# Performance work log

Hardware: AMD Instinct MI355X
Metric: run time of the kernel (lower is better)

Reference implementation:

```python
import jax, jax.numpy as jnp
import numpy as np

N_NODES = 50000
N_EDGES = 800000
IN_DIM = 128
HID_DIM = 128
OUT_DIM = 64


def setup_inputs() -> dict:
    key = jax.random.key(0)
    ks = jax.random.split(key, 6)
    x = jax.random.normal(ks[0], (N_NODES, IN_DIM), dtype=jnp.float32)
    row = jax.random.randint(ks[1], (N_EDGES,), 0, N_NODES, dtype=jnp.int32)
    col = jax.random.randint(ks[2], (N_EDGES,), 0, N_NODES, dtype=jnp.int32)
    vals = jax.random.uniform(ks[3], (N_EDGES,), dtype=jnp.float32)
    # Xavier-uniform init as in nn.init.xavier_uniform_
    lim1 = float(np.sqrt(6.0 / (IN_DIM + HID_DIM)))
    lim2 = float(np.sqrt(6.0 / (HID_DIM + OUT_DIM)))
    W1 = jax.random.uniform(ks[4], (IN_DIM, HID_DIM), minval=-lim1, maxval=lim1, dtype=jnp.float32)
    W2 = jax.random.uniform(ks[5], (HID_DIM, OUT_DIM), minval=-lim2, maxval=lim2, dtype=jnp.float32)
    return {"x": x, "row": row, "col": col, "vals": vals, "W1": W1, "W2": W2}


def _spmm(row, col, vals, x):
    # out[i] = sum_{e: row[e]==i} vals[e] * x[col[e]]   (sparse adj @ x)
    msgs = vals[:, None] * x[col]  # [E, D] gathered edge messages
    return jax.ops.segment_sum(msgs, row, num_segments=N_NODES)


def reference(x, row, col, vals, W1, W2):
    # GCN layer 1: adj.mm(x) -> linear -> relu  (dropout = identity in eval)
    h = jax.nn.relu(_spmm(row, col, vals, x) @ W1)
    # GCN layer 2: adj.mm(h) -> linear (no activation)
    out = _spmm(row, col, vals, h) @ W2
    return out
```

## Files before the change

kernel.cpp:

```cpp
#include <hip/hip_runtime.h>
#include <stdint.h>

#define N_NODES 50000
#define N_EDGES 800000
#define IN_DIM 128
#define HID_DIM 128
#define OUT_DIM 64

#define ELL_CAP 64
#define XCD_GROUPS 8
#define ROWS_PER_XCD (N_NODES / XCD_GROUPS)
#define SCAT_BLOCKS_PER_XCD 128

typedef short bf16x8 __attribute__((ext_vector_type(8)));
typedef float f32x4  __attribute__((ext_vector_type(4)));

__device__ __forceinline__ uint32_t pack_bf16x2(float a, float b) {
    uint32_t ba = __float_as_uint(a), bb = __float_as_uint(b);
    ba = (ba + 0x7fffu + ((ba >> 16) & 1u)) >> 16;
    bb = (bb + 0x7fffu + ((bb >> 16) & 1u)) & 0xffff0000u;
    return ba | bb;
}

__device__ __forceinline__ unsigned short f2bf(float f) {
    uint32_t u = __float_as_uint(f);
    return (unsigned short)((u + 0x7fffu + ((u >> 16) & 1u)) >> 16);
}

__device__ __forceinline__ uint32_t pack_edge(int col, float v) {
    uint32_t fb = __float_as_uint(v);
    fb = (fb + 0x7fffu + ((fb >> 16) & 1u)) & 0xffff0000u;
    return fb | (uint32_t)col;
}


__global__ __launch_bounds__(256) void zero_convert(int* __restrict__ counts,
                                                    const float* __restrict__ W1,
                                                    const float* __restrict__ W2,
                                                    unsigned short* __restrict__ wt1,
                                                    unsigned short* __restrict__ wt2) {
    int i = blockIdx.x * 256 + threadIdx.x;
    if (i < N_NODES) counts[i] = 0;
    int j = i - N_NODES;
    if (j >= 0 && j < 128 * 128) {
        int n = j >> 7, k = j & 127;
        wt1[j] = f2bf(W1[k * 128 + n]);
    }
    int l = j - 128 * 128;
    if (l >= 0 && l < 64 * 128) {
        int n = l >> 7, k = l & 127;
        wt2[l] = f2bf(W2[k * 64 + n]);
    }
}


__global__ __launch_bounds__(256) void scatter_ell(const int* __restrict__ row,
                                                   const int* __restrict__ col,
                                                   const float* __restrict__ vals,
                                                   int* __restrict__ counts,
                                                   uint32_t* __restrict__ ell) {
    const int xcd = blockIdx.x & (XCD_GROUPS - 1);
    const int blk = blockIdx.x >> 3;
    const int rlo = xcd * ROWS_PER_XCD;
    int e = blk * 256 + threadIdx.x;
    const int stride = SCAT_BLOCKS_PER_XCD * 256;
    for (; e < N_EDGES; e += stride) {
        int r = row[e];
        if ((unsigned)(r - rlo) < (unsigned)ROWS_PER_XCD) {
            int p = atomicAdd(&counts[r], 1);
            if (p < ELL_CAP)
                ell[((size_t)r << 6) + p] = pack_edge(col[e], vals[e]);
        }
    }
}


template<int N, bool AF32>
__global__ __launch_bounds__(256) void gemm_mfma(const float* __restrict__ Af,
                                                 const uint32_t* __restrict__ Apk,
                                                 const unsigned short* __restrict__ Wt,
                                                 unsigned short* __restrict__ outb) {
    const int tid = threadIdx.x;
    const int wid = tid >> 6, lane = tid & 63;
    const int l15 = lane & 15, lk = lane >> 4;
    const int n0 = blockIdx.y * 64;

    bf16x8 bfrag[4][4];
#pragma unroll
    for (int t = 0; t < 4; ++t) {
        const unsigned short* wp = Wt + (size_t)(n0 + t * 16 + l15) * 128 + lk * 8;
#pragma unroll
        for (int s = 0; s < 4; ++s)
            bfrag[t][s] = *reinterpret_cast<const bf16x8*>(wp + s * 32);
    }

    for (int mt = blockIdx.x * 4 + wid; mt < 3125; mt += 784) {
        const int row = mt * 16 + l15;
        bf16x8 afrag[4];
        if (AF32) {
            const float* ap = Af + (size_t)row * 128 + lk * 8;
#pragma unroll
            for (int s = 0; s < 4; ++s) {
                float4 p0 = *reinterpret_cast<const float4*>(ap + s * 32);
                float4 p1 = *reinterpret_cast<const float4*>(ap + s * 32 + 4);
                bf16x8 f;
                f[0] = (short)f2bf(p0.x); f[1] = (short)f2bf(p0.y);
                f[2] = (short)f2bf(p0.z); f[3] = (short)f2bf(p0.w);
                f[4] = (short)f2bf(p1.x); f[5] = (short)f2bf(p1.y);
                f[6] = (short)f2bf(p1.z); f[7] = (short)f2bf(p1.w);
                afrag[s] = f;
            }
        } else {
            const uint32_t* ap = Apk + (size_t)row * 64 + lk * 4;
#pragma unroll
            for (int s = 0; s < 4; ++s)
                afrag[s] = *reinterpret_cast<const bf16x8*>(ap + s * 16);
        }

        f32x4 acc[4] = {{0.f,0.f,0.f,0.f},{0.f,0.f,0.f,0.f},{0.f,0.f,0.f,0.f},{0.f,0.f,0.f,0.f}};
#pragma unroll
        for (int s = 0; s < 4; ++s)
#pragma unroll
            for (int t = 0; t < 4; ++t)
                acc[t] = __builtin_amdgcn_mfma_f32_16x16x32_bf16(afrag[s], bfrag[t][s], acc[t], 0, 0, 0);

#pragma unroll
        for (int t = 0; t < 4; ++t)
#pragma unroll
            for (int q = 0; q < 4; ++q) {
                int r = mt * 16 + lk * 4 + q;
                outb[(size_t)r * N + n0 + t * 16 + l15] = f2bf(acc[t][q]);
            }
    }
}


template<bool RELU>
__global__ __launch_bounds__(256) void spmm_bf16_128(const int* __restrict__ counts,
                                                     const uint32_t* __restrict__ ell,
                                                     const uint32_t* __restrict__ xp,
                                                     uint32_t* __restrict__ outp) {
    const int wid = threadIdx.x >> 6;
    const int lane = threadIdx.x & 63;
    const int r = blockIdx.x * 4 + wid;
    if (r >= N_NODES) return;
    const int start = r << 6;
    int cnt = counts[r]; if (cnt > ELL_CAP) cnt = ELL_CAP;
    const int end = start + cnt;
    const uint32_t* xb = xp + lane;

    float alo[4] = {0.f, 0.f, 0.f, 0.f};
    float ahi[4] = {0.f, 0.f, 0.f, 0.f};
    int e = start;
    for (; e + 7 < end; e += 8) {
        uint32_t c0 = ell[e],     c1 = ell[e + 1], c2 = ell[e + 2], c3 = ell[e + 3];
        uint32_t c4 = ell[e + 4], c5 = ell[e + 5], c6 = ell[e + 6], c7 = ell[e + 7];
        uint32_t u0 = xb[(size_t)(c0 & 0xffffu) * 64];
        uint32_t u1 = xb[(size_t)(c1 & 0xffffu) * 64];
        uint32_t u2 = xb[(size_t)(c2 & 0xffffu) * 64];
        uint32_t u3 = xb[(size_t)(c3 & 0xffffu) * 64];
        uint32_t u4 = xb[(size_t)(c4 & 0xffffu) * 64];
        uint32_t u5 = xb[(size_t)(c5 & 0xffffu) * 64];
        uint32_t u6 = xb[(size_t)(c6 & 0xffffu) * 64];
        uint32_t u7 = xb[(size_t)(c7 & 0xffffu) * 64];
        float v0 = __uint_as_float(c0 & 0xffff0000u), v1 = __uint_as_float(c1 & 0xffff0000u);
        float v2 = __uint_as_float(c2 & 0xffff0000u), v3 = __uint_as_float(c3 & 0xffff0000u);
        float v4 = __uint_as_float(c4 & 0xffff0000u), v5 = __uint_as_float(c5 & 0xffff0000u);
        float v6 = __uint_as_float(c6 & 0xffff0000u), v7 = __uint_as_float(c7 & 0xffff0000u);
        alo[0] = fmaf(v0, __uint_as_float(u0 << 16), alo[0]);
        ahi[0] = fmaf(v0, __uint_as_float(u0 & 0xffff0000u), ahi[0]);
        alo[1] = fmaf(v1, __uint_as_float(u1 << 16), alo[1]);
        ahi[1] = fmaf(v1, __uint_as_float(u1 & 0xffff0000u), ahi[1]);
        alo[2] = fmaf(v2, __uint_as_float(u2 << 16), alo[2]);
        ahi[2] = fmaf(v2, __uint_as_float(u2 & 0xffff0000u), ahi[2]);
        alo[3] = fmaf(v3, __uint_as_float(u3 << 16), alo[3]);
        ahi[3] = fmaf(v3, __uint_as_float(u3 & 0xffff0000u), ahi[3]);
        alo[0] = fmaf(v4, __uint_as_float(u4 << 16), alo[0]);
        ahi[0] = fmaf(v4, __uint_as_float(u4 & 0xffff0000u), ahi[0]);
        alo[1] = fmaf(v5, __uint_as_float(u5 << 16), alo[1]);
        ahi[1] = fmaf(v5, __uint_as_float(u5 & 0xffff0000u), ahi[1]);
        alo[2] = fmaf(v6, __uint_as_float(u6 << 16), alo[2]);
        ahi[2] = fmaf(v6, __uint_as_float(u6 & 0xffff0000u), ahi[2]);
        alo[3] = fmaf(v7, __uint_as_float(u7 << 16), alo[3]);
        ahi[3] = fmaf(v7, __uint_as_float(u7 & 0xffff0000u), ahi[3]);
    }
    if (e + 3 < end) {
        uint32_t c0 = ell[e], c1 = ell[e + 1], c2 = ell[e + 2], c3 = ell[e + 3];
        uint32_t u0 = xb[(size_t)(c0 & 0xffffu) * 64];
        uint32_t u1 = xb[(size_t)(c1 & 0xffffu) * 64];
        uint32_t u2 = xb[(size_t)(c2 & 0xffffu) * 64];
        uint32_t u3 = xb[(size_t)(c3 & 0xffffu) * 64];
        float v0 = __uint_as_float(c0 & 0xffff0000u), v1 = __uint_as_float(c1 & 0xffff0000u);
        float v2 = __uint_as_float(c2 & 0xffff0000u), v3 = __uint_as_float(c3 & 0xffff0000u);
        alo[0] = fmaf(v0, __uint_as_float(u0 << 16), alo[0]);
        ahi[0] = fmaf(v0, __uint_as_float(u0 & 0xffff0000u), ahi[0]);
        alo[1] = fmaf(v1, __uint_as_float(u1 << 16), alo[1]);
        ahi[1] = fmaf(v1, __uint_as_float(u1 & 0xffff0000u), ahi[1]);
        alo[2] = fmaf(v2, __uint_as_float(u2 << 16), alo[2]);
        ahi[2] = fmaf(v2, __uint_as_float(u2 & 0xffff0000u), ahi[2]);
        alo[3] = fmaf(v3, __uint_as_float(u3 << 16), alo[3]);
        ahi[3] = fmaf(v3, __uint_as_float(u3 & 0xffff0000u), ahi[3]);
        e += 4;
    }
    for (; e < end; ++e) {
        uint32_t c0 = ell[e];
        float v0 = __uint_as_float(c0 & 0xffff0000u);
        uint32_t u0 = xb[(size_t)(c0 & 0xffffu) * 64];
        alo[0] = fmaf(v0, __uint_as_float(u0 << 16), alo[0]);
        ahi[0] = fmaf(v0, __uint_as_float(u0 & 0xffff0000u), ahi[0]);
    }
    float rlo = (alo[0] + alo[1]) + (alo[2] + alo[3]);
    float rhi = (ahi[0] + ahi[1]) + (ahi[2] + ahi[3]);
    if (RELU) { rlo = fmaxf(rlo, 0.f); rhi = fmaxf(rhi, 0.f); }
    outp[(size_t)r * 64 + lane] = pack_bf16x2(rlo, rhi);
}

__global__ __launch_bounds__(256) void spmm_bf16_64(const int* __restrict__ counts,
                                                    const uint32_t* __restrict__ ell,
                                                    const uint32_t* __restrict__ xp,
                                                    float* __restrict__ out) {
    const int wid = threadIdx.x >> 6;
    const int lane = threadIdx.x & 63;
    const int r = blockIdx.x * 4 + wid;
    if (r >= N_NODES) return;
    const int start = r << 6;
    int cnt = counts[r]; if (cnt > ELL_CAP) cnt = ELL_CAP;
    const int end = start + cnt;
    const int j = lane & 31;
    const int half = lane >> 5;
    const uint32_t* xb = xp + j;

    float alo[4] = {0.f, 0.f, 0.f, 0.f};
    float ahi[4] = {0.f, 0.f, 0.f, 0.f};
    int e = start + half;
    for (; e + 6 < end; e += 8) {
        uint32_t c0 = ell[e], c1 = ell[e + 2], c2 = ell[e + 4], c3 = ell[e + 6];
        uint32_t u0 = xb[(size_t)(c0 & 0xffffu) * 32];
        uint32_t u1 = xb[(size_t)(c1 & 0xffffu) * 32];
        uint32_t u2 = xb[(size_t)(c2 & 0xffffu) * 32];
        uint32_t u3 = xb[(size_t)(c3 & 0xffffu) * 32];
        float v0 = __uint_as_float(c0 & 0xffff0000u), v1 = __uint_as_float(c1 & 0xffff0000u);
        float v2 = __uint_as_float(c2 & 0xffff0000u), v3 = __uint_as_float(c3 & 0xffff0000u);
        alo[0] = fmaf(v0, __uint_as_float(u0 << 16), alo[0]);
        ahi[0] = fmaf(v0, __uint_as_float(u0 & 0xffff0000u), ahi[0]);
        alo[1] = fmaf(v1, __uint_as_float(u1 << 16), alo[1]);
        ahi[1] = fmaf(v1, __uint_as_float(u1 & 0xffff0000u), ahi[1]);
        alo[2] = fmaf(v2, __uint_as_float(u2 << 16), alo[2]);
        ahi[2] = fmaf(v2, __uint_as_float(u2 & 0xffff0000u), ahi[2]);
        alo[3] = fmaf(v3, __uint_as_float(u3 << 16), alo[3]);
        ahi[3] = fmaf(v3, __uint_as_float(u3 & 0xffff0000u), ahi[3]);
    }
    for (; e < end; e += 2) {
        uint32_t c0 = ell[e];
        float v = __uint_as_float(c0 & 0xffff0000u);
        uint32_t u = xb[(size_t)(c0 & 0xffffu) * 32];
        alo[0] = fmaf(v, __uint_as_float(u << 16), alo[0]);
        ahi[0] = fmaf(v, __uint_as_float(u & 0xffff0000u), ahi[0]);
    }
    float alo_s = (alo[0] + alo[1]) + (alo[2] + alo[3]);
    float ahi_s = (ahi[0] + ahi[1]) + (ahi[2] + ahi[3]);
    alo_s += __shfl_xor(alo_s, 32);
    ahi_s += __shfl_xor(ahi_s, 32);
    if (half == 0) {
        float2 res = {alo_s, ahi_s};
        *reinterpret_cast<float2*>(out + (size_t)r * 64 + j * 2) = res;
    }
}


extern "C" void kernel_launch(void* const* d_in, const int* in_sizes, int n_in,
                              void* d_out, int out_size, void* d_ws, size_t ws_size,
                              hipStream_t stream) {
    const float* x    = (const float*)d_in[0];
    const int*   row  = (const int*)  d_in[1];
    const int*   col  = (const int*)  d_in[2];
    const float* vals = (const float*)d_in[3];
    const float* W1   = (const float*)d_in[4];
    const float* W2   = (const float*)d_in[5];
    float* out = (float*)d_out;

    char* ws = (char*)d_ws;
    auto align = [](size_t v) { return (v + 255) & ~(size_t)255; };
    int*      counts  = (int*)ws;              ws += align(sizeof(int) * N_NODES);
    uint32_t* ell     = (uint32_t*)ws;         ws += align(sizeof(uint32_t) * N_NODES * ELL_CAP);
    uint32_t* tpk     = (uint32_t*)ws;         ws += align(sizeof(uint32_t) * N_NODES * 64);
    uint32_t* hpk     = (uint32_t*)ws;         ws += align(sizeof(uint32_t) * N_NODES * 64);
    unsigned short* wt1 = (unsigned short*)ws; ws += align(sizeof(short) * 128 * 128);
    unsigned short* wt2 = (unsigned short*)ws; ws += align(sizeof(short) * 64 * 128);

    zero_convert<<<(N_NODES + 128 * 128 + 64 * 128 + 255) / 256, 256, 0, stream>>>(counts, W1, W2, wt1, wt2);
    scatter_ell<<<SCAT_BLOCKS_PER_XCD * XCD_GROUPS, 256, 0, stream>>>(row, col, vals, counts, ell);

    gemm_mfma<HID_DIM, true><<<dim3(196, 2), 256, 0, stream>>>(x, nullptr, wt1, (unsigned short*)tpk);
    spmm_bf16_128<true><<<(N_NODES + 3) / 4, 256, 0, stream>>>(counts, ell, tpk, hpk);

    gemm_mfma<OUT_DIM, false><<<dim3(196, 1), 256, 0, stream>>>(nullptr, hpk, wt2, (unsigned short*)tpk);
    spmm_bf16_64<<<(N_NODES + 3) / 4, 256, 0, stream>>>(counts, ell, tpk, out);
}
```

Baseline: 130.6 us.

## Fuse ELL scatter with first GEMM and store layer-1 features as FP8

Merges the edge-scatter kernel and the first MFMA GEMM into one launch by splitting the block range, so the two independent stages can run concurrently. The first GEMM now writes its output as custom FP8 (e4m3-like) bytes instead of bf16, and the first SpMM gathers 2 bytes per lane and decodes them through a shared-memory lookup table. This halves the gather traffic of the dominant sparse stage and removes one kernel launch, at the cost of reduced precision in the intermediate features and extra LDS lookups.

```diff
diff --git a/kernel.cpp b/kernel.cpp
--- a/kernel.cpp
+++ b/kernel.cpp
@@ -11,6 +11,8 @@
 #define XCD_GROUPS 8
 #define ROWS_PER_XCD (N_NODES / XCD_GROUPS)
 #define SCAT_BLOCKS_PER_XCD 128
+#define SCAT_BLOCKS (SCAT_BLOCKS_PER_XCD * XCD_GROUPS)
+#define GEMM1_BLOCKS 392
 
 typedef short bf16x8 __attribute__((ext_vector_type(8)));
 typedef float f32x4  __attribute__((ext_vector_type(4)));
@@ -25,6 +27,20 @@
 __device__ __forceinline__ unsigned short f2bf(float f) {
     uint32_t u = __float_as_uint(f);
     return (unsigned short)((u + 0x7fffu + ((u >> 16) & 1u)) >> 16);
+}
+
+__device__ __forceinline__ uint8_t f2fp8(float f) {
+    uint32_t u = __float_as_uint(f);
+    uint32_t s = (u >> 24) & 0x80u;
+    uint32_t au = u & 0x7fffffffu;
+    uint32_t r = au + 0x7FFFFu + ((au >> 20) & 1u);
+    int e = (int)((r >> 23) & 0xffu) - 120;
+    uint32_t m = (r >> 20) & 7u;
+    uint32_t out;
+    if (e <= 0) out = 0u;
+    else if (e >= 16) out = 0x7Eu;
+    else out = ((uint32_t)e << 3) | m;
+    return (uint8_t)(s | out);
 }
 
 __device__ __forceinline__ uint32_t pack_edge(int col, float v) {
@@ -54,67 +70,61 @@
 }
 
 
-__global__ __launch_bounds__(256) void scatter_ell(const int* __restrict__ row,
-                                                   const int* __restrict__ col,
-                                                   const float* __restrict__ vals,
-                                                   int* __restrict__ counts,
-                                                   uint32_t* __restrict__ ell) {
-    const int xcd = blockIdx.x & (XCD_GROUPS - 1);
-    const int blk = blockIdx.x >> 3;
-    const int rlo = xcd * ROWS_PER_XCD;
-    int e = blk * 256 + threadIdx.x;
-    const int stride = SCAT_BLOCKS_PER_XCD * 256;
-    for (; e < N_EDGES; e += stride) {
-        int r = row[e];
-        if ((unsigned)(r - rlo) < (unsigned)ROWS_PER_XCD) {
-            int p = atomicAdd(&counts[r], 1);
-            if (p < ELL_CAP)
-                ell[((size_t)r << 6) + p] = pack_edge(col[e], vals[e]);
+__global__ __launch_bounds__(256) void fused_scatter_gemm1(const int* __restrict__ row,
+                                                           const int* __restrict__ col,
+                                                           const float* __restrict__ vals,
+                                                           int* __restrict__ counts,
+                                                           uint32_t* __restrict__ ell,
+                                                           const float* __restrict__ x,
+                                                           const unsigned short* __restrict__ wt1,
+                                                           uint8_t* __restrict__ t1f8) {
+    if (blockIdx.x < SCAT_BLOCKS) {
+        const int xcd = blockIdx.x & (XCD_GROUPS - 1);
+        const int blk = blockIdx.x >> 3;
+        const int rlo = xcd * ROWS_PER_XCD;
+        int e = blk * 256 + threadIdx.x;
+        const int stride = SCAT_BLOCKS_PER_XCD * 256;
+        for (; e < N_EDGES; e += stride) {
+            int r = row[e];
+            if ((unsigned)(r - rlo) < (unsigned)ROWS_PER_XCD) {
+                int p = atomicAdd(&counts[r], 1);
+                if (p < ELL_CAP)
+                    ell[((size_t)r << 6) + p] = pack_edge(col[e], vals[e]);
+            }
         }
-    }
-}
-
-
-template<int N, bool AF32>
-__global__ __launch_bounds__(256) void gemm_mfma(const float* __restrict__ Af,
-                                                 const uint32_t* __restrict__ Apk,
-                                                 const unsigned short* __restrict__ Wt,
-                                                 unsigned short* __restrict__ outb) {
+        return;
+    }
+
+    const int g  = blockIdx.x - SCAT_BLOCKS;
+    const int bx = g % 196;
+    const int n0 = (g / 196) * 64;
     const int tid = threadIdx.x;
     const int wid = tid >> 6, lane = tid & 63;
     const int l15 = lane & 15, lk = lane >> 4;
-    const int n0 = blockIdx.y * 64;
 
     bf16x8 bfrag[4][4];
 #pragma unroll
     for (int t = 0; t < 4; ++t) {
-        const unsigned short* wp = Wt + (size_t)(n0 + t * 16 + l15) * 128 + lk * 8;
+        const unsigned short* wp = wt1 + (size_t)(n0 + t * 16 + l15) * 128 + lk * 8;
 #pragma unroll
         for (int s = 0; s < 4; ++s)
             bfrag[t][s] = *reinterpret_cast<const bf16x8*>(wp + s * 32);
     }
 
-    for (int mt = blockIdx.x * 4 + wid; mt < 3125; mt += 784) {
-        const int row = mt * 16 + l15;
+    for (int mt = bx * 4 + wid; mt < 3125; mt += 784) {
+        const int arow = mt * 16 + l15;
         bf16x8 afrag[4];
-        if (AF32) {
-            const float* ap = Af + (size_t)row * 128 + lk * 8;
-#pragma unroll
-            for (int s = 0; s < 4; ++s) {
-                float4 p0 = *reinterpret_cast<const float4*>(ap + s * 32);
-                float4 p1 = *reinterpret_cast<const float4*>(ap + s * 32 + 4);
-                bf16x8 f;
-                f[0] = (short)f2bf(p0.x); f[1] = (short)f2bf(p0.y);
-                f[2] = (short)f2bf(p0.z); f[3] = (short)f2bf(p0.w);
-                f[4] = (short)f2bf(p1.x); f[5] = (short)f2bf(p1.y);
-                f[6] = (short)f2bf(p1.z); f[7] = (short)f2bf(p1.w);
-                afrag[s] = f;
-            }
-        } else {
-            const uint32_t* ap = Apk + (size_t)row * 64 + lk * 4;
-#pragma unroll
-            for (int s = 0; s < 4; ++s)
-                afrag[s] = *reinterpret_cast<const bf16x8*>(ap + s * 16);
+        const float* ap = x + (size_t)arow * 128 + lk * 8;
+#pragma unroll
+        for (int s = 0; s < 4; ++s) {
+            float4 p0 = *reinterpret_cast<const float4*>(ap + s * 32);
+            float4 p1 = *reinterpret_cast<const float4*>(ap + s * 32 + 4);
+            bf16x8 f;
+            f[0] = (short)f2bf(p0.x); f[1] = (short)f2bf(p0.y);
+            f[2] = (short)f2bf(p0.z); f[3] = (short)f2bf(p0.w);
+            f[4] = (short)f2bf(p1.x); f[5] = (short)f2bf(p1.y);
+            f[6] = (short)f2bf(p1.z); f[7] = (short)f2bf(p1.w);
+            afrag[s] = f;
         }
 
         f32x4 acc[4] = {{0.f,0.f,0.f,0.f},{0.f,0.f,0.f,0.f},{0.f,0.f,0.f,0.f},{0.f,0.f,0.f,0.f}};
@@ -129,17 +139,68 @@
 #pragma unroll
             for (int q = 0; q < 4; ++q) {
                 int r = mt * 16 + lk * 4 + q;
-                outb[(size_t)r * N + n0 + t * 16 + l15] = f2bf(acc[t][q]);
+                t1f8[(size_t)r * 128 + n0 + t * 16 + l15] = f2fp8(acc[t][q]);
             }
     }
 }
 
 
+__global__ __launch_bounds__(256) void gemm_mfma2(const uint32_t* __restrict__ Apk,
+                                                  const unsigned short* __restrict__ Wt,
+                                                  unsigned short* __restrict__ outb) {
+    const int tid = threadIdx.x;
+    const int wid = tid >> 6, lane = tid & 63;
+    const int l15 = lane & 15, lk = lane >> 4;
+
+    bf16x8 bfrag[4][4];
+#pragma unroll
+    for (int t = 0; t < 4; ++t) {
+        const unsigned short* wp = Wt + (size_t)(t * 16 + l15) * 128 + lk * 8;
+#pragma unroll
+        for (int s = 0; s < 4; ++s)
+            bfrag[t][s] = *reinterpret_cast<const bf16x8*>(wp + s * 32);
+    }
+
+    for (int mt = blockIdx.x * 4 + wid; mt < 3125; mt += 784) {
+        const int arow = mt * 16 + l15;
+        bf16x8 afrag[4];
+        const uint32_t* ap = Apk + (size_t)arow * 64 + lk * 4;
+#pragma unroll
+        for (int s = 0; s < 4; ++s)
+            afrag[s] = *reinterpret_cast<const bf16x8*>(ap + s * 16);
+
+        f32x4 acc[4] = {{0.f,0.f,0.f,0.f},{0.f,0.f,0.f,0.f},{0.f,0.f,0.f,0.f},{0.f,0.f,0.f,0.f}};
+#pragma unroll
+        for (int s = 0; s < 4; ++s)
+#pragma unroll
+            for (int t = 0; t < 4; ++t)
+                acc[t] = __builtin_amdgcn_mfma_f32_16x16x32_bf16(afrag[s], bfrag[t][s], acc[t], 0, 0, 0);
+
+#pragma unroll
+        for (int t = 0; t < 4; ++t)
+#pragma unroll
+            for (int q = 0; q < 4; ++q) {
+                int r = mt * 16 + lk * 4 + q;
+                outb[(size_t)r * 64 + t * 16 + l15] = f2bf(acc[t][q]);
+            }
+    }
+}
+
+
 template<bool RELU>
-__global__ __launch_bounds__(256) void spmm_bf16_128(const int* __restrict__ counts,
-                                                     const uint32_t* __restrict__ ell,
-                                                     const uint32_t* __restrict__ xp,
-                                                     uint32_t* __restrict__ outp) {
+__global__ __launch_bounds__(256) void spmm_fp8_128(const int* __restrict__ counts,
+                                                    const uint32_t* __restrict__ ell,
+                                                    const uint8_t* __restrict__ x8,
+                                                    uint32_t* __restrict__ outp) {
+    __shared__ float lut[256];
+    {
+        int b = threadIdx.x;
+        uint32_t ee = (b >> 3) & 15u, mm = b & 7u;
+        float f = (ee == 0) ? ldexpf((float)mm, -9) : ldexpf((float)(8 + mm), (int)ee - 10);
+        lut[b] = (b & 0x80) ? -f : f;
+    }
+    __syncthreads();
+
     const int wid = threadIdx.x >> 6;
     const int lane = threadIdx.x & 63;
     const int r = blockIdx.x * 4 + wid;
@@ -147,7 +208,7 @@
     const int start = r << 6;
     int cnt = counts[r]; if (cnt > ELL_CAP) cnt = ELL_CAP;
     const int end = start + cnt;
-    const uint32_t* xb = xp + lane;
+    const uint8_t* xb = x8 + lane * 2;
 
     float alo[4] = {0.f, 0.f, 0.f, 0.f};
     float ahi[4] = {0.f, 0.f, 0.f, 0.f};
@@ -155,65 +216,53 @@
     for (; e + 7 < end; e += 8) {
         uint32_t c0 = ell[e],     c1 = ell[e + 1], c2 = ell[e + 2], c3 = ell[e + 3];
         uint32_t c4 = ell[e + 4], c5 = ell[e + 5], c6 = ell[e + 6], c7 = ell[e + 7];
-        uint32_t u0 = xb[(size_t)(c0 & 0xffffu) * 64];
-        uint32_t u1 = xb[(size_t)(c1 & 0xffffu) * 64];
-        uint32_t u2 = xb[(size_t)(c2 & 0xffffu) * 64];
-        uint32_t u3 = xb[(size_t)(c3 & 0xffffu) * 64];
-        uint32_t u4 = xb[(size_t)(c4 & 0xffffu) * 64];
-        uint32_t u5 = xb[(size_t)(c5 & 0xffffu) * 64];
-        uint32_t u6 = xb[(size_t)(c6 & 0xffffu) * 64];
-        uint32_t u7 = xb[(size_t)(c7 & 0xffffu) * 64];
+        unsigned short u0 = *reinterpret_cast<const unsigned short*>(xb + (size_t)(c0 & 0xffffu) * 128);
+        unsigned short u1 = *reinterpret_cast<const unsigned short*>(xb + (size_t)(c1 & 0xffffu) * 128);
+        unsigned short u2 = *reinterpret_cast<const unsigned short*>(xb + (size_t)(c2 & 0xffffu) * 128);
+        unsigned short u3 = *reinterpret_cast<const unsigned short*>(xb + (size_t)(c3 & 0xffffu) * 128);
+        unsigned short u4 = *reinterpret_cast<const unsigned short*>(xb + (size_t)(c4 & 0xffffu) * 128);
+        unsigned short u5 = *reinterpret_cast<const unsigned short*>(xb + (size_t)(c5 & 0xffffu) * 128);
+        unsigned short u6 = *reinterpret_cast<const unsigned short*>(xb + (size_t)(c6 & 0xffffu) * 128);
+        unsigned short u7 = *reinterpret_cast<const unsigned short*>(xb + (size_t)(c7 & 0xffffu) * 128);
         float v0 = __uint_as_float(c0 & 0xffff0000u), v1 = __uint_as_float(c1 & 0xffff0000u);
         float v2 = __uint_as_float(c2 & 0xffff0000u), v3 = __uint_as_float(c3 & 0xffff0000u);
         float v4 = __uint_as_float(c4 & 0xffff0000u), v5 = __uint_as_float(c5 & 0xffff0000u);
         float v6 = __uint_as_float(c6 & 0xffff0000u), v7 = __uint_as_float(c7 & 0xffff0000u);
-        alo[0] = fmaf(v0, __uint_as_float(u0 << 16), alo[0]);
-        ahi[0] = fmaf(v0, __uint_as_float(u0 & 0xffff0000u), ahi[0]);
-        alo[1] = fmaf(v1, __uint_as_float(u1 << 16), alo[1]);
-        ahi[1] = fmaf(v1, __uint_as_float(u1 & 0xffff0000u), ahi[1]);
-        alo[2] = fmaf(v2, __uint_as_float(u2 << 16), alo[2]);
-        ahi[2] = fmaf(v2, __uint_as_float(u2 & 0xffff0000u), ahi[2]);
-        alo[3] = fmaf(v3, __uint_as_float(u3 << 16), alo[3]);
-        ahi[3] = fmaf(v3, __uint_as_float(u3 & 0xffff0000u), ahi[3]);
-        alo[0] = fmaf(v4, __uint_as_float(u4 << 16), alo[0]);
-        ahi[0] = fmaf(v4, __uint_as_float(u4 & 0xffff0000u), ahi[0]);
-        alo[1] = fmaf(v5, __uint_as_float(u5 << 16), alo[1]);
-        ahi[1] = fmaf(v5, __uint_as_float(u5 & 0xffff0000u), ahi[1]);
-        alo[2] = fmaf(v6, __uint_as_float(u6 << 16), alo[2]);
-        ahi[2] = fmaf(v6, __uint_as_float(u6 & 0xffff0000u), ahi[2]);
-        alo[3] = fmaf(v7, __uint_as_float(u7 << 16), alo[3]);
-        ahi[3] = fmaf(v7, __uint_as_float(u7 & 0xffff0000u), ahi[3]);
+        alo[0] = fmaf(v0, lut[u0 & 0xff], alo[0]); ahi[0] = fmaf(v0, lut[u0 >> 8], ahi[0]);
+        alo[1] = fmaf(v1, lut[u1 & 0xff], alo[1]); ahi[1] = fmaf(v1, lut[u1 >> 8], ahi[1]);
+        alo[2] = fmaf(v2, lut[u2 & 0xff], alo[2]); ahi[2] = fmaf(v2, lut[u2 >> 8], ahi[2]);
+        alo[3] = fmaf(v3, lut[u3 & 0xff], alo[3]); ahi[3] = fmaf(v3, lut[u3 >> 8], ahi[3]);
+        alo[0] = fmaf(v4, lut[u4 & 0xff], alo[0]); ahi[0] = fmaf(v4, lut[u4 >> 8], ahi[0]);
+        alo[1] = fmaf(v5, lut[u5 & 0xff], alo[1]); ahi[1] = fmaf(v5, lut[u5 >> 8], ahi[1]);
+        alo[2] = fmaf(v6, lut[u6 & 0xff], alo[2]); ahi[2] = fmaf(v6, lut[u6 >> 8], ahi[2]);
+        alo[3] = fmaf(v7, lut[u7 & 0xff], alo[3]); ahi[3] = fmaf(v7, lut[u7 >> 8], ahi[3]);
     }
     if (e + 3 < end) {
         uint32_t c0 = ell[e], c1 = ell[e + 1], c2 = ell[e + 2], c3 = ell[e + 3];
-        uint32_t u0 = xb[(size_t)(c0 & 0xffffu) * 64];
-        uint32_t u1 = xb[(size_t)(c1 & 0xffffu) * 64];
-        uint32_t u2 = xb[(size_t)(c2 & 0xffffu) * 64];
-        uint32_t u3 = xb[(size_t)(c3 & 0xffffu) * 64];
+        unsigned short u0 = *reinterpret_cast<const unsigned short*>(xb + (size_t)(c0 & 0xffffu) * 128);
+        unsigned short u1 = *reinterpret_cast<const unsigned short*>(xb + (size_t)(c1 & 0xffffu) * 128);
+        unsigned short u2 = *reinterpret_cast<const unsigned short*>(xb + (size_t)(c2 & 0xffffu) * 128);
+        unsigned short u3 = *reinterpret_cast<const unsigned short*>(xb + (size_t)(c3 & 0xffffu) * 128);
         float v0 = __uint_as_float(c0 & 0xffff0000u), v1 = __uint_as_float(c1 & 0xffff0000u);
         float v2 = __uint_as_float(c2 & 0xffff0000u), v3 = __uint_as_float(c3 & 0xffff0000u);
-        alo[0] = fmaf(v0, __uint_as_float(u0 << 16), alo[0]);
-        ahi[0] = fmaf(v0, __uint_as_float(u0 & 0xffff0000u), ahi[0]);
-        alo[1] = fmaf(v1, __uint_as_float(u1 << 16), alo[1]);
-        ahi[1] = fmaf(v1, __uint_as_float(u1 & 0xffff0000u), ahi[1]);
-        alo[2] = fmaf(v2, __uint_as_float(u2 << 16), alo[2]);
-        ahi[2] = fmaf(v2, __uint_as_float(u2 & 0xffff0000u), ahi[2]);
-        alo[3] = fmaf(v3, __uint_as_float(u3 << 16), alo[3]);
-        ahi[3] = fmaf(v3, __uint_as_float(u3 & 0xffff0000u), ahi[3]);
+        alo[0] = fmaf(v0, lut[u0 & 0xff], alo[0]); ahi[0] = fmaf(v0, lut[u0 >> 8], ahi[0]);
+        alo[1] = fmaf(v1, lut[u1 & 0xff], alo[1]); ahi[1] = fmaf(v1, lut[u1 >> 8], ahi[1]);
+        alo[2] = fmaf(v2, lut[u2 & 0xff], alo[2]); ahi[2] = fmaf(v2, lut[u2 >> 8], ahi[2]);
+        alo[3] = fmaf(v3, lut[u3 & 0xff], alo[3]); ahi[3] = fmaf(v3, lut[u3 >> 8], ahi[3]);
         e += 4;
     }
     for (; e < end; ++e) {
         uint32_t c0 = ell[e];
         float v0 = __uint_as_float(c0 & 0xffff0000u);
-        uint32_t u0 = xb[(size_t)(c0 & 0xffffu) * 64];
-        alo[0] = fmaf(v0, __uint_as_float(u0 << 16), alo[0]);
-        ahi[0] = fmaf(v0, __uint_as_float(u0 & 0xffff0000u), ahi[0]);
+        unsigned short u0 = *reinterpret_cast<const unsigned short*>(xb + (size_t)(c0 & 0xffffu) * 128);
+        alo[0] = fmaf(v0, lut[u0 & 0xff], alo[0]); ahi[0] = fmaf(v0, lut[u0 >> 8], ahi[0]);
     }
     float rlo = (alo[0] + alo[1]) + (alo[2] + alo[3]);
     float rhi = (ahi[0] + ahi[1]) + (ahi[2] + ahi[3]);
     if (RELU) { rlo = fmaxf(rlo, 0.f); rhi = fmaxf(rhi, 0.f); }
     outp[(size_t)r * 64 + lane] = pack_bf16x2(rlo, rhi);
 }
+
 
 __global__ __launch_bounds__(256) void spmm_bf16_64(const int* __restrict__ counts,
                                                     const uint32_t* __restrict__ ell,
@@ -283,17 +332,19 @@
     auto align = [](size_t v) { return (v + 255) & ~(size_t)255; };
     int*      counts  = (int*)ws;              ws += align(sizeof(int) * N_NODES);
     uint32_t* ell     = (uint32_t*)ws;         ws += align(sizeof(uint32_t) * N_NODES * ELL_CAP);
-    uint32_t* tpk     = (uint32_t*)ws;         ws += align(sizeof(uint32_t) * N_NODES * 64);
+    uint8_t*  t1f8    = (uint8_t*)ws;          ws += align(sizeof(uint8_t) * N_NODES * 128);
     uint32_t* hpk     = (uint32_t*)ws;         ws += align(sizeof(uint32_t) * N_NODES * 64);
+    uint32_t* tpk     = (uint32_t*)ws;         ws += align(sizeof(uint32_t) * N_NODES * 32);
     unsigned short* wt1 = (unsigned short*)ws; ws += align(sizeof(short) * 128 * 128);
     unsigned short* wt2 = (unsigned short*)ws; ws += align(sizeof(short) * 64 * 128);
 
     zero_convert<<<(N_NODES + 128 * 128 + 64 * 128 + 255) / 256, 256, 0, stream>>>(counts, W1, W2, wt1, wt2);
-    scatter_ell<<<SCAT_BLOCKS_PER_XCD * XCD_GROUPS, 256, 0, stream>>>(row, col, vals, counts, ell);
-
-    gemm_mfma<HID_DIM, true><<<dim3(196, 2), 256, 0, stream>>>(x, nullptr, wt1, (unsigned short*)tpk);
-    spmm_bf16_128<true><<<(N_NODES + 3) / 4, 256, 0, stream>>>(counts, ell, tpk, hpk);
-
-    gemm_mfma<OUT_DIM, false><<<dim3(196, 1), 256, 0, stream>>>(nullptr, hpk, wt2, (unsigned short*)tpk);
+
+    fused_scatter_gemm1<<<SCAT_BLOCKS + GEMM1_BLOCKS, 256, 0, stream>>>(
+        row, col, vals, counts, ell, x, wt1, t1f8);
+
+    spmm_fp8_128<true><<<(N_NODES + 3) / 4, 256, 0, stream>>>(counts, ell, t1f8, hpk);
+
+    gemm_mfma2<<<196, 256, 0, stream>>>(hpk, wt2, (unsigned short*)tpk);
     spmm_bf16_64<<<(N_NODES + 3) / 4, 256, 0, stream>>>(counts, ell, tpk, out);
 }
```

Result: slower. 133.9 us (+2.5%).
